# Performance work log

Measured on AMD Instinct MI355X. Metric: run time of the kernel, lower is better.

The kernel has to match this reference:

```python
import jax, jax.numpy as jnp
import numpy as np

B, S, K, N = 4, 2048, 4096, 4096


def setup_inputs() -> dict:
    key = jax.random.key(0)
    k1, k2, k3, k4 = jax.random.split(key, 4)
    x = jax.random.normal(k1, (B, S, K), dtype=jnp.float32)
    # int8 quantized weight values in [-128, 127], stored as int32 (jax-friendly container)
    qw = jax.random.randint(k2, (N, K), -128, 128, dtype=jnp.int32)
    # per-tensor scale: amax/127 style scalar
    sw = (jax.random.uniform(k3, (), dtype=jnp.float32) * 0.02 + 0.001)
    bias = jax.random.normal(k4, (N,), dtype=jnp.float32)
    return {"x": x, "qw": qw, "sw": sw, "bias": bias}


def reference(x, qw, sw, bias):
    # per_tensor_matmul: dequantize weight to fp32 with scalar scale, fp32 GEMM, cast back, add bias
    x_dtype = x.dtype
    w = qw.astype(jnp.float32) * sw          # [N, K] dequantized
    y = jnp.einsum('bsk,nk->bsn', x.astype(jnp.float32), w).astype(x_dtype)
    y = y + bias                              # [B, S, N]
    return y
```

## Files before the change

kernel.cpp:

```cpp
#include <hip/hip_runtime.h>
#include <stdint.h>

#define MDIM 8192
#define NDIM 4096
#define KDIM 4096

#define BM 256
#define BN 256
#define BK 128
#define NKT (KDIM / BK)

typedef __attribute__((ext_vector_type(4)))  int i32x4;

#define AS1 __attribute__((address_space(1)))
#define AS3 __attribute__((address_space(3)))

__device__ __forceinline__ int clamp127(int v) {
    return v > 127 ? 127 : (v < -127 ? -127 : v);
}

__global__ __launch_bounds__(256) void quant_x(
        const float* __restrict__ x, const float* __restrict__ sw,
        int8_t* __restrict__ Aq, float* __restrict__ scales) {
    const int row = blockIdx.x;
    const int t   = threadIdx.x;
    const float4* px = (const float4*)(x + (size_t)row * KDIM);

    float4 v[4];
#pragma unroll
    for (int j = 0; j < 4; j++) v[j] = px[t + 256 * j];

    float a = 0.f;
#pragma unroll
    for (int j = 0; j < 4; j++) {
        a = fmaxf(a, fabsf(v[j].x)); a = fmaxf(a, fabsf(v[j].y));
        a = fmaxf(a, fabsf(v[j].z)); a = fmaxf(a, fabsf(v[j].w));
    }
#pragma unroll
    for (int off = 32; off >= 1; off >>= 1)
        a = fmaxf(a, __shfl_xor(a, off));
    __shared__ float red[4];
    if ((t & 63) == 0) red[t >> 6] = a;
    __syncthreads();
    const float amax = fmaxf(fmaxf(red[0], red[1]), fmaxf(red[2], red[3]));
    const float inv  = (amax > 0.f) ? (127.0f / amax) : 0.f;
    if (t == 0) scales[row] = (amax * (1.0f / 127.0f)) * (*sw);

    int* out32 = (int*)(Aq + (size_t)row * KDIM);
#pragma unroll
    for (int j = 0; j < 4; j++) {
        int b0 = clamp127(__float2int_rn(v[j].x * inv));
        int b1 = clamp127(__float2int_rn(v[j].y * inv));
        int b2 = clamp127(__float2int_rn(v[j].z * inv));
        int b3 = clamp127(__float2int_rn(v[j].w * inv));
        out32[t + 256 * j] = (b0 & 255) | ((b1 & 255) << 8) | ((b2 & 255) << 16) | ((b3 & 255) << 24);
    }
}

__global__ __launch_bounds__(256) void cvt_w(const int* __restrict__ qw, int8_t* __restrict__ Bq) {
    const long i = (long)blockIdx.x * 256 + threadIdx.x;
    int4 a = ((const int4*)qw)[i];
    ((int*)Bq)[i] = (a.x & 255) | ((a.y & 255) << 8) | ((a.z & 255) << 16) | ((a.w & 255) << 24);
}


#define BAR()    do { asm volatile("" ::: "memory"); __builtin_amdgcn_s_barrier(); asm volatile("" ::: "memory"); } while (0)
#define WAITV(n) asm volatile("s_waitcnt vmcnt(" #n ")" ::: "memory")

#define STAGE_A(buf, h, kt) do { \
    __builtin_amdgcn_global_load_lds((AS1 const void*)(gA + (size_t)((h) * 128) * KDIM + (kt) * 128), \
        (AS3 void*)(sA + (buf) * 32768 + (h) * 16384 + sdst), 16, 0, 0); \
    __builtin_amdgcn_global_load_lds((AS1 const void*)(gA + (size_t)((h) * 128 + 64) * KDIM + (kt) * 128), \
        (AS3 void*)(sA + (buf) * 32768 + (h) * 16384 + 8192 + sdst), 16, 0, 0); \
} while (0)

#define STAGE_B(buf, h, kt) do { \
    __builtin_amdgcn_global_load_lds((AS1 const void*)(gB + (size_t)((h) * 128) * KDIM + (kt) * 128), \
        (AS3 void*)(sB + (buf) * 32768 + (h) * 16384 + sdst), 16, 0, 0); \
    __builtin_amdgcn_global_load_lds((AS1 const void*)(gB + (size_t)((h) * 128 + 64) * KDIM + (kt) * 128), \
        (AS3 void*)(sB + (buf) * 32768 + (h) * 16384 + 8192 + sdst), 16, 0, 0); \
} while (0)

#define READ_A0(buf) do { \
    _Pragma("unroll") for (int mi = 0; mi < 4; ++mi) \
    _Pragma("unroll") for (int ks = 0; ks < 2; ++ks) \
        aF0[mi][ks] = *(const i32x4*)(sA + (buf) * 32768 + rbA + mi * 2048 + co[ks]); \
} while (0)

#define READ_A1(buf) do { \
    _Pragma("unroll") for (int mi = 0; mi < 4; ++mi) \
    _Pragma("unroll") for (int ks = 0; ks < 2; ++ks) \
        aF1[mi][ks] = *(const i32x4*)(sA + (buf) * 32768 + rbA + (4 + mi) * 2048 + co[ks]); \
} while (0)

#define READ_Bb(buf) do { \
    _Pragma("unroll") for (int ni = 0; ni < 4; ++ni) \
    _Pragma("unroll") for (int ks = 0; ks < 2; ++ks) \
        bF[ni][ks] = *(const i32x4*)(sB + (buf) * 32768 + rbB + ni * 2048 + co[ks]); \
} while (0)

#define MMA0(nh) do { \
    __builtin_amdgcn_s_setprio(1); \
    _Pragma("unroll") for (int ks = 0; ks < 2; ++ks) \
    _Pragma("unroll") for (int mi = 0; mi < 4; ++mi) \
    _Pragma("unroll") for (int nj = 0; nj < 2; ++nj) \
        acc[mi][2 * (nh) + nj] = __builtin_amdgcn_mfma_i32_16x16x64_i8( \
            aF0[mi][ks], bF[2 * (nh) + nj][ks], acc[mi][2 * (nh) + nj], 0, 0, 0); \
    __builtin_amdgcn_s_setprio(0); \
} while (0)

#define MMA1(nh) do { \
    __builtin_amdgcn_s_setprio(1); \
    _Pragma("unroll") for (int ks = 0; ks < 2; ++ks) \
    _Pragma("unroll") for (int mi = 0; mi < 4; ++mi) \
    _Pragma("unroll") for (int nj = 0; nj < 2; ++nj) \
        acc[4 + mi][2 * (nh) + nj] = __builtin_amdgcn_mfma_i32_16x16x64_i8( \
            aF1[mi][ks], bF[2 * (nh) + nj][ks], acc[4 + mi][2 * (nh) + nj], 0, 0, 0); \
    __builtin_amdgcn_s_setprio(0); \
} while (0)

__global__ __launch_bounds__(512, 2) void gemm_bt_i8(
        const int8_t* __restrict__ A,
        const int8_t* __restrict__ Bm,
        const float* __restrict__ scales,
        const float* __restrict__ bias,
        float* __restrict__ C)
{
    __shared__ __align__(16) int8_t sA[2 * BM * BK];
    __shared__ __align__(16) int8_t sB[2 * BN * BK];

    const int tid  = threadIdx.x;
    const int wave = tid >> 6;
    const int lane = tid & 63;
    const int wr   = wave >> 2;
    const int wc   = wave & 3;
    const int lr   = lane & 15;
    const int lg   = lane >> 4;

    const int orig = blockIdx.y * 16 + blockIdx.x;
    const int nu   = (orig & 7) * 64 + (orig >> 3);
    const int m0   = (nu >> 4) * BM;
    const int n0   = (nu & 15) * BN;

    const int trow = tid >> 3;
    const int slog = (tid & 7) ^ (((tid >> 5) & 1) << 1);
    const int8_t* gA = A  + (size_t)(m0 + trow) * KDIM + slog * 16;
    const int8_t* gB = Bm + (size_t)(n0 + trow) * KDIM + slog * 16;
    const int sdst = tid * 16;

    const int f = ((lr >> 2) & 1) << 1;
    const int rbA = (wr * 128 + lr) * BK;
    const int rbB = (wc * 64  + lr) * BK;
    int co[2];
#pragma unroll
    for (int ks = 0; ks < 2; ++ks) co[ks] = ks * 64 + ((lg ^ f) << 4);

    i32x4 acc[8][4];
#pragma unroll
    for (int mi = 0; mi < 8; ++mi)
#pragma unroll
        for (int ni = 0; ni < 4; ++ni)
#pragma unroll
            for (int r = 0; r < 4; ++r) acc[mi][ni][r] = 0;

    i32x4 aF0[4][2];
    i32x4 aF1[4][2];
    i32x4 bF[4][2];

    STAGE_B(0, 0, 0); STAGE_B(0, 1, 0);
    STAGE_A(0, 0, 0); STAGE_A(0, 1, 0);
    STAGE_B(1, 0, 1); STAGE_B(1, 1, 1);
    STAGE_A(1, 0, 1); STAGE_A(1, 1, 1);
    WAITV(8);
    BAR();

#pragma unroll 1
    for (int it = 0; it < NKT / 2 - 1; ++it) {
        const int t2 = 2 * it + 2, t3 = 2 * it + 3;
        READ_A0(0); READ_Bb(0);                    BAR(); MMA0(0); BAR();
        READ_A1(0);                                BAR(); MMA0(1); BAR();
        STAGE_B(0, 0, t2);                         BAR(); MMA1(1); BAR();
        STAGE_B(0, 1, t2); WAITV(4);               BAR(); MMA1(0); BAR();
        READ_A0(1); READ_Bb(1);
        STAGE_A(0, 0, t2); STAGE_A(0, 1, t2);      BAR(); MMA0(0); BAR();
        READ_A1(1);                                BAR(); MMA0(1); BAR();
        STAGE_B(1, 0, t3); STAGE_B(1, 1, t3);      BAR(); MMA1(1); BAR();
        STAGE_A(1, 0, t3); STAGE_A(1, 1, t3); WAITV(8); BAR(); MMA1(0); BAR();
    }

    READ_A0(0); READ_Bb(0);                        BAR(); MMA0(0); BAR();
    READ_A1(0);                                    BAR(); MMA0(1); BAR();
                                                   BAR(); MMA1(1); BAR();
    WAITV(0);                                      BAR(); MMA1(0); BAR();
    READ_A0(1); READ_Bb(1);                        BAR(); MMA0(0); BAR();
    READ_A1(1);                                    BAR(); MMA0(1); BAR();
    MMA1(1);
    MMA1(0);

#pragma unroll
    for (int mi = 0; mi < 8; ++mi) {
        const int row_base = m0 + wr * 128 + mi * 16 + lg * 4;
        float sc[4];
#pragma unroll
        for (int r = 0; r < 4; ++r) sc[r] = scales[row_base + r];
#pragma unroll
        for (int ni = 0; ni < 4; ++ni) {
            const int col = n0 + wc * 64 + ni * 16 + lr;
            const float bc = bias[col];
#pragma unroll
            for (int r = 0; r < 4; ++r)
                C[(size_t)(row_base + r) * NDIM + col] = (float)acc[mi][ni][r] * sc[r] + bc;
        }
    }
}

__global__ void gemm_naive_f32(const float* __restrict__ x, const int* __restrict__ qw,
                               const float* __restrict__ sw, const float* __restrict__ bias,
                               float* __restrict__ out) {
    size_t id = (size_t)blockIdx.x * blockDim.x + threadIdx.x;
    if (id >= (size_t)MDIM * NDIM) return;
    int m = (int)(id / NDIM);
    int n = (int)(id % NDIM);
    const float* xr = x + (size_t)m * KDIM;
    const int*   wr = qw + (size_t)n * KDIM;
    float acc = 0.f;
    for (int k = 0; k < KDIM; k++) acc += xr[k] * (float)wr[k];
    out[id] = acc * (*sw) + bias[n];
}

extern "C" void kernel_launch(void* const* d_in, const int* in_sizes, int n_in,
                              void* d_out, int out_size, void* d_ws, size_t ws_size,
                              hipStream_t stream) {
    const float* x    = (const float*)d_in[0];
    const int*   qw   = (const int*)d_in[1];
    const float* sw   = (const float*)d_in[2];
    const float* bias = (const float*)d_in[3];
    float* out = (float*)d_out;

    const size_t needA = (size_t)MDIM * KDIM;
    const size_t needB = (size_t)NDIM * KDIM;
    const size_t needS = (size_t)MDIM * sizeof(float);

    if (ws_size >= needA + needB + needS) {
        int8_t* Aq = (int8_t*)d_ws;
        int8_t* Bq = Aq + needA;
        float*  scales = (float*)(Bq + needB);

        quant_x<<<MDIM, 256, 0, stream>>>(x, sw, Aq, scales);
        const long nw4 = (long)NDIM * KDIM / 4;
        cvt_w<<<(int)(nw4 / 256), 256, 0, stream>>>(qw, Bq);

        dim3 grid(NDIM / BN, MDIM / BM);
        gemm_bt_i8<<<grid, 512, 0, stream>>>(Aq, Bq, scales, bias, out);
    } else {
        size_t total = (size_t)MDIM * NDIM;
        gemm_naive_f32<<<(total + 255) / 256, 256, 0, stream>>>(x, qw, sw, bias, out);
    }
}
```

Measured before the change: 405.7 us.

## Restructure int8 GEMM main loop into a ping-pong schedule overlapping LDS reads with MFMA

Rewrites the main K loop so that LDS fragment reads for the next sub-step are issued alongside the current MFMA block. Barriers drop from two per MFMA block to one. B fragments are split into two halves to reduce register pressure, and the global-to-LDS staging order and vmcnt waits are rescheduled to interleave A and B stages across buffers. The aim is to hide LDS latency and barrier stalls behind matrix-core work. The cost is a more delicate dependency schedule where wrong wait counts could race on shared buffers.

```diff
diff --git a/kernel.cpp b/kernel.cpp
--- a/kernel.cpp
+++ b/kernel.cpp
@@ -65,6 +65,7 @@
 
 
 #define BAR()    do { asm volatile("" ::: "memory"); __builtin_amdgcn_s_barrier(); asm volatile("" ::: "memory"); } while (0)
+#define LGKM0()  asm volatile("s_waitcnt lgkmcnt(0)" ::: "memory")
 #define WAITV(n) asm volatile("s_waitcnt vmcnt(" #n ")" ::: "memory")
 
 #define STAGE_A(buf, h, kt) do { \
@@ -93,29 +94,25 @@
         aF1[mi][ks] = *(const i32x4*)(sA + (buf) * 32768 + rbA + (4 + mi) * 2048 + co[ks]); \
 } while (0)
 
-#define READ_Bb(buf) do { \
-    _Pragma("unroll") for (int ni = 0; ni < 4; ++ni) \
-    _Pragma("unroll") for (int ks = 0; ks < 2; ++ks) \
-        bF[ni][ks] = *(const i32x4*)(sB + (buf) * 32768 + rbB + ni * 2048 + co[ks]); \
-} while (0)
-
-#define MMA0(nh) do { \
+#define READ_B01(buf) do { \
+    _Pragma("unroll") for (int ni = 0; ni < 2; ++ni) \
+    _Pragma("unroll") for (int ks = 0; ks < 2; ++ks) \
+        bF01[ni][ks] = *(const i32x4*)(sB + (buf) * 32768 + rbB + ni * 2048 + co[ks]); \
+} while (0)
+
+#define READ_B23(buf) do { \
+    _Pragma("unroll") for (int ni = 0; ni < 2; ++ni) \
+    _Pragma("unroll") for (int ks = 0; ks < 2; ++ks) \
+        bF23[ni][ks] = *(const i32x4*)(sB + (buf) * 32768 + rbB + (2 + ni) * 2048 + co[ks]); \
+} while (0)
+
+#define MMA_(AF, accbase, BF, nhofs) do { \
     __builtin_amdgcn_s_setprio(1); \
     _Pragma("unroll") for (int ks = 0; ks < 2; ++ks) \
     _Pragma("unroll") for (int mi = 0; mi < 4; ++mi) \
     _Pragma("unroll") for (int nj = 0; nj < 2; ++nj) \
-        acc[mi][2 * (nh) + nj] = __builtin_amdgcn_mfma_i32_16x16x64_i8( \
-            aF0[mi][ks], bF[2 * (nh) + nj][ks], acc[mi][2 * (nh) + nj], 0, 0, 0); \
-    __builtin_amdgcn_s_setprio(0); \
-} while (0)
-
-#define MMA1(nh) do { \
-    __builtin_amdgcn_s_setprio(1); \
-    _Pragma("unroll") for (int ks = 0; ks < 2; ++ks) \
-    _Pragma("unroll") for (int mi = 0; mi < 4; ++mi) \
-    _Pragma("unroll") for (int nj = 0; nj < 2; ++nj) \
-        acc[4 + mi][2 * (nh) + nj] = __builtin_amdgcn_mfma_i32_16x16x64_i8( \
-            aF1[mi][ks], bF[2 * (nh) + nj][ks], acc[4 + mi][2 * (nh) + nj], 0, 0, 0); \
+        acc[(accbase) + mi][(nhofs) + nj] = __builtin_amdgcn_mfma_i32_16x16x64_i8( \
+            AF[mi][ks], BF[nj][ks], acc[(accbase) + mi][(nhofs) + nj], 0, 0, 0); \
     __builtin_amdgcn_s_setprio(0); \
 } while (0)
 
@@ -165,37 +162,37 @@
 
     i32x4 aF0[4][2];
     i32x4 aF1[4][2];
-    i32x4 bF[4][2];
-
+    i32x4 bF01[2][2];
+    i32x4 bF23[2][2];
+
+    STAGE_A(0, 0, 0); STAGE_A(0, 1, 0);
     STAGE_B(0, 0, 0); STAGE_B(0, 1, 0);
-    STAGE_A(0, 0, 0); STAGE_A(0, 1, 0);
-    STAGE_B(1, 0, 1); STAGE_B(1, 1, 1);
     STAGE_A(1, 0, 1); STAGE_A(1, 1, 1);
-    WAITV(8);
+    WAITV(4);
     BAR();
+    READ_A0(0); READ_B01(0);
 
 #pragma unroll 1
     for (int it = 0; it < NKT / 2 - 1; ++it) {
-        const int t2 = 2 * it + 2, t3 = 2 * it + 3;
-        READ_A0(0); READ_Bb(0);                    BAR(); MMA0(0); BAR();
-        READ_A1(0);                                BAR(); MMA0(1); BAR();
-        STAGE_B(0, 0, t2);                         BAR(); MMA1(1); BAR();
-        STAGE_B(0, 1, t2); WAITV(4);               BAR(); MMA1(0); BAR();
-        READ_A0(1); READ_Bb(1);
-        STAGE_A(0, 0, t2); STAGE_A(0, 1, t2);      BAR(); MMA0(0); BAR();
-        READ_A1(1);                                BAR(); MMA0(1); BAR();
-        STAGE_B(1, 0, t3); STAGE_B(1, 1, t3);      BAR(); MMA1(1); BAR();
-        STAGE_A(1, 0, t3); STAGE_A(1, 1, t3); WAITV(8); BAR(); MMA1(0); BAR();
-    }
-
-    READ_A0(0); READ_Bb(0);                        BAR(); MMA0(0); BAR();
-    READ_A1(0);                                    BAR(); MMA0(1); BAR();
-                                                   BAR(); MMA1(1); BAR();
-    WAITV(0);                                      BAR(); MMA1(0); BAR();
-    READ_A0(1); READ_Bb(1);                        BAR(); MMA0(0); BAR();
-    READ_A1(1);                                    BAR(); MMA0(1); BAR();
-    MMA1(1);
-    MMA1(0);
+        const int e = 2 * it;
+        READ_A1(0);                 MMA_(aF0, 0, bF01, 0); STAGE_B(1, 0, e + 1); BAR();
+        READ_B23(0);                MMA_(aF1, 4, bF01, 0); STAGE_B(1, 1, e + 1); LGKM0(); BAR();
+                                    MMA_(aF0, 0, bF23, 2); STAGE_A(0, 0, e + 2); WAITV(2); BAR();
+        READ_A0(1); READ_B01(1);    MMA_(aF1, 4, bF23, 2); STAGE_A(0, 1, e + 2); BAR();
+        READ_A1(1);                 MMA_(aF0, 0, bF01, 0); STAGE_B(0, 0, e + 2); BAR();
+        READ_B23(1);                MMA_(aF1, 4, bF01, 0); STAGE_B(0, 1, e + 2); LGKM0(); BAR();
+                                    MMA_(aF0, 0, bF23, 2); STAGE_A(1, 0, e + 3); WAITV(2); BAR();
+        READ_A0(0); READ_B01(0);    MMA_(aF1, 4, bF23, 2); STAGE_A(1, 1, e + 3); BAR();
+    }
+
+    READ_A1(0);                 MMA_(aF0, 0, bF01, 0); STAGE_B(1, 0, 31); BAR();
+    READ_B23(0);                MMA_(aF1, 4, bF01, 0); STAGE_B(1, 1, 31); LGKM0(); BAR();
+                                MMA_(aF0, 0, bF23, 2); WAITV(0); BAR();
+    READ_A0(1); READ_B01(1);    MMA_(aF1, 4, bF23, 2); BAR();
+    READ_A1(1);                 MMA_(aF0, 0, bF01, 0); BAR();
+    READ_B23(1);                MMA_(aF1, 4, bF01, 0); BAR();
+                                MMA_(aF0, 0, bF23, 2);
+                                MMA_(aF1, 4, bF23, 2);
 
 #pragma unroll
     for (int mi = 0; mi < 8; ++mi) {
```

New measurement: 402.4 us. No clear change (-0.8%).
